# Performance work log

Measured on AMD Instinct MI355X. Metric: run time of the kernel, lower is better.

## Reference

```python
import jax, jax.numpy as jnp
import numpy as np

B, T, C = 8, 2048, 1024
HS, HO = 64, 64  # head_size, head_output_dim

def setup_inputs() -> dict:
    key = jax.random.key(0)
    k1, k2, k3, k4 = jax.random.split(key, 4)
    x = jax.random.normal(k1, (B, T, C), dtype=jnp.float32)
    Wk = jax.random.normal(k2, (HS, C), dtype=jnp.float32) * (C ** -0.5)
    Wq = jax.random.normal(k3, (HS, C), dtype=jnp.float32) * (C ** -0.5)
    Wv = jax.random.normal(k4, (HO, C), dtype=jnp.float32) * (C ** -0.5)
    return {"x": x, "Wk": Wk, "Wq": Wq, "Wv": Wv}

def reference(x, Wk, Wq, Wv):
    Bx, Tx, Cx = x.shape
    k = jnp.einsum('btc,hc->bth', x, Wk)  # [B,T,HS]
    q = jnp.einsum('btc,hc->bth', x, Wq)  # [B,T,HS]
    v = jnp.einsum('btc,oc->bto', x, Wv)  # [B,T,HO]
    scores = jnp.einsum('bth,bsh->bts', q, k)  # [B,T,T]
    causal = jnp.tril(jnp.ones((Tx, Tx), dtype=bool))
    scores = jnp.where(causal, scores, -jnp.inf)
    # original scales AFTER masking; -inf * scale stays -inf, same softmax result
    weights = jax.nn.softmax(scores * (HS ** -0.5), axis=-1)
    return jnp.einsum('bts,bso->bto', weights, v)
```

## Files before the change

kernel.cpp:

```cpp
#include <hip/hip_runtime.h>
#include <hip/hip_bf16.h>

typedef __attribute__((ext_vector_type(8))) short short8;
typedef __attribute__((ext_vector_type(4))) float float4v;

#define LOG2E 1.44269504088896340736f

typedef __attribute__((address_space(1))) const unsigned int gu32;
typedef __attribute__((address_space(3))) unsigned int su32;

__device__ __forceinline__ unsigned short f2bf(float f) {
    unsigned int u = __float_as_uint(f);
    unsigned int r = (u + 0x7fffu + ((u >> 16) & 1u)) >> 16;
    return (unsigned short)r;
}

__global__ void wconv_kernel(const float* __restrict__ Wk, const float* __restrict__ Wq,
                             const float* __restrict__ Wv, unsigned short* __restrict__ Wb) {
    int i = blockIdx.x * 256 + threadIdx.x;
    if (i >= 192 * 1024) return;
    float v;
    if (i < 65536)       v = Wk[i];
    else if (i < 131072) v = Wq[i - 65536];
    else                 v = Wv[i - 131072];
    Wb[i] = f2bf(v);
}

__global__ __launch_bounds__(256) void proj_kernel(
    const float* __restrict__ x, const unsigned short* __restrict__ Wb,
    unsigned short* __restrict__ qs, unsigned short* __restrict__ ks,
    unsigned short* __restrict__ vT) {
    __shared__ unsigned short Bl[3][12288];

    const int tid  = threadIdx.x;
    const int lane = tid & 63;
    const int wave = tid >> 6;
    const int rg   = wave & 1;
    const int g    = wave >> 1;
    const int quad = lane >> 4;
    const int l16  = lane & 15;
    const int t0   = blockIdx.x * 32;

    const int srow_in = lane >> 3;
    const int csrc    = (lane & 7) ^ srow_in;

    const int rowA = t0 + rg * 16 + l16;
    const float* xr = x + (size_t)rowA * 1024;

    float4v acc[6];
#pragma unroll
    for (int n = 0; n < 6; n++) acc[n] = (float4v){0.f, 0.f, 0.f, 0.f};

#define STAGE_B(BUF, KN)                                                          \
    {                                                                             \
        _Pragma("unroll")                                                         \
        for (int i = 0; i < 6; i++) {                                             \
            const int region = wave * 6 + i;                                      \
            const int rowg   = region * 8 + srow_in;                              \
            const unsigned short* src = Wb + (size_t)rowg * 1024 + (KN) + csrc * 8; \
            __builtin_amdgcn_global_load_lds((gu32*)src,                          \
                                             (su32*)&Bl[BUF][region * 512],       \
                                             16, 0, 0);                           \
        }                                                                         \
    }

#define LOAD_A(DST, KN)                                             \
    {                                                               \
        DST[0] = *(const float4v*)(xr + (KN) + quad * 8);           \
        DST[1] = *(const float4v*)(xr + (KN) + quad * 8 + 4);       \
        DST[2] = *(const float4v*)(xr + (KN) + 32 + quad * 8);      \
        DST[3] = *(const float4v*)(xr + (KN) + 32 + quad * 8 + 4);  \
    }

    STAGE_B(0, 0)
    asm volatile("" ::: "memory");
    float4v a0[4], a1[4];
    LOAD_A(a0, 0)
    asm volatile("" ::: "memory");
    STAGE_B(1, 64)
    asm volatile("" ::: "memory");
    LOAD_A(a1, 64)

    const int swz = l16 & 7;

#pragma unroll
    for (int kt = 0; kt < 16; kt++) {
        __builtin_amdgcn_sched_barrier(0);
        if (kt < 15) {
            asm volatile("s_waitcnt vmcnt(10)" ::: "memory");
        } else {
            asm volatile("s_waitcnt vmcnt(0)" ::: "memory");
        }
        __builtin_amdgcn_s_barrier();
        if (kt < 14) {
            STAGE_B((kt + 2) % 3, (kt + 2) * 64)
            asm volatile("" ::: "memory");
        }
        float4v an[4];
        if (kt < 14) {
            LOAD_A(an, (kt + 2) * 64)
            asm volatile("" ::: "memory");
        }
        const unsigned short* Bc = Bl[kt % 3];
#pragma unroll
        for (int kc = 0; kc < 2; kc++) {
            short8 af;
#pragma unroll
            for (int j = 0; j < 4; j++) af[j] = (short)f2bf(a0[kc * 2][j]);
#pragma unroll
            for (int j = 0; j < 4; j++) af[4 + j] = (short)f2bf(a0[kc * 2 + 1][j]);
#pragma unroll
            for (int n = 0; n < 6; n++) {
                const int row  = (g * 6 + n) * 16 + l16;
                const int coff = ((kc * 4 + quad) ^ swz) * 8;
                const short8 bf = *(const short8*)&Bc[row * 64 + coff];
                acc[n] = __builtin_amdgcn_mfma_f32_16x16x32_bf16(af, bf, acc[n], 0, 0, 0);
            }
        }
        if (kt < 14) {
#pragma unroll
            for (int i = 0; i < 4; i++) { a0[i] = a1[i]; a1[i] = an[i]; }
        } else if (kt < 15) {
#pragma unroll
            for (int i = 0; i < 4; i++) a0[i] = a1[i];
        }
    }
#undef STAGE_B
#undef LOAD_A

    const int rowD = t0 + rg * 16 + quad * 4;
#pragma unroll
    for (int r = 0; r < 4; r++) {
        const int t = rowD + r;
        const int b = t >> 11, tt = t & 2047;
        if (g == 0) {
#pragma unroll
            for (int n = 0; n < 4; n++)
                ks[(size_t)t * 64 + n * 16 + l16] = f2bf(acc[n][r]);
#pragma unroll
            for (int n = 4; n < 6; n++)
                qs[(size_t)t * 64 + (n - 4) * 16 + l16] = f2bf(acc[n][r] * 0.125f);
        } else {
#pragma unroll
            for (int n = 0; n < 2; n++)
                qs[(size_t)t * 64 + (n + 2) * 16 + l16] = f2bf(acc[n][r] * 0.125f);
#pragma unroll
            for (int n = 2; n < 6; n++)
                vT[(size_t)b * 131072 + (size_t)((n - 2) * 16 + l16) * 2048 + tt] = f2bf(acc[n][r]);
        }
    }
}

__global__ __launch_bounds__(256) void attn_kernel(
    const unsigned short* __restrict__ qs, const unsigned short* __restrict__ ks,
    const unsigned short* __restrict__ vT, float* __restrict__ out) {
    __shared__ unsigned short Kl[4 * 64 * 72];
    __shared__ unsigned short Vl[64 * 264];
    __shared__ unsigned short P[4][16 * 72];
    __shared__ float Ll[4][16];
    float* Of = (float*)Kl;

    const int tid  = threadIdx.x;
    const int lane = tid & 63;
    const int wave = tid >> 6;
    const int quad = lane >> 4;
    const int l16  = lane & 15;
    const int bx   = blockIdx.x;
    const int b    = bx & 7;
    const int i    = bx >> 3;
    const int qt   = (i & 1) ? (127 - (i >> 1)) : (i >> 1);
    const int t0   = qt * 16;

    const unsigned short* qb = qs + (size_t)b * 131072;
    const unsigned short* kb = ks + (size_t)b * 131072;
    const unsigned short* vb = vT + (size_t)b * 131072;

    const int ksr = tid >> 3;
    const int ksc = (tid & 7) * 8;
    const int vsr = tid >> 5;
    const int vsc = (tid & 31) * 8;

    const int qrow = t0 + l16;
    const short8 qf0 = *(const short8*)(qb + (size_t)qrow * 64 + quad * 8);
    const short8 qf1 = *(const short8*)(qb + (size_t)qrow * 64 + 32 + quad * 8);

    float4v o[4];
#pragma unroll
    for (int ot = 0; ot < 4; ot++) o[ot] = (float4v){0.f, 0.f, 0.f, 0.f};
    float lpart = 0.f;

    const int nkb  = (qt >> 2) + 1;
    const int nsup = (nkb + 3) >> 2;

    for (int s = 0; s < nsup; s++) {
        const int key0 = s * 256;
        __syncthreads();
#pragma unroll
        for (int i2 = 0; i2 < 8; i2++) {
            int kr = key0 + i2 * 32 + ksr; kr = kr < 2047 ? kr : 2047;
            *(short8*)&Kl[(i2 * 32 + ksr) * 72 + ksc] = *(const short8*)(kb + (size_t)kr * 64 + ksc);
        }
#pragma unroll
        for (int i2 = 0; i2 < 8; i2++) {
            const int orow = i2 * 8 + vsr;
            int kc2 = key0 + vsc; kc2 = kc2 < 2040 ? kc2 : 2040;
            *(short8*)&Vl[orow * 264 + vsc] = *(const short8*)(vb + (size_t)orow * 2048 + kc2);
        }
        __syncthreads();

        const int jt = s * 4 + wave;
        if (jt < nkb) {
            const int kbase = wave * 64;
            float4v sv[4];
#pragma unroll
            for (int kt = 0; kt < 4; kt++) {
                const short8 ka = *(const short8*)&Kl[(kbase + kt * 16 + l16) * 72 + quad * 8];
                const short8 kc = *(const short8*)&Kl[(kbase + kt * 16 + l16) * 72 + 32 + quad * 8];
                float4v z = (float4v){0.f, 0.f, 0.f, 0.f};
                z = __builtin_amdgcn_mfma_f32_16x16x32_bf16(ka, qf0, z, 0, 0, 0);
                sv[kt] = __builtin_amdgcn_mfma_f32_16x16x32_bf16(kc, qf1, z, 0, 0, 0);
            }
            if (jt == nkb - 1) {
#pragma unroll
                for (int kt = 0; kt < 4; kt++)
#pragma unroll
                    for (int r = 0; r < 4; r++)
                        if (jt * 64 + kt * 16 + quad * 4 + r > qrow) sv[kt][r] = -1e30f;
            }
#pragma unroll
            for (int kt = 0; kt < 4; kt++) {
                float p0 = exp2f(sv[kt][0] * LOG2E);
                float p1 = exp2f(sv[kt][1] * LOG2E);
                float p2 = exp2f(sv[kt][2] * LOG2E);
                float p3 = exp2f(sv[kt][3] * LOG2E);
                lpart += (p0 + p1) + (p2 + p3);
                unsigned int lo = (unsigned int)f2bf(p0) | ((unsigned int)f2bf(p1) << 16);
                unsigned int hi = (unsigned int)f2bf(p2) | ((unsigned int)f2bf(p3) << 16);
                unsigned long long w = ((unsigned long long)hi << 32) | lo;
                *(unsigned long long*)&P[wave][l16 * 72 + kt * 16 + quad * 4] = w;
            }
#pragma unroll
            for (int kc = 0; kc < 2; kc++) {
                const short8 pf = *(const short8*)&P[wave][l16 * 72 + kc * 32 + quad * 8];
#pragma unroll
                for (int ot = 0; ot < 4; ot++) {
                    const short8 vf = *(const short8*)&Vl[(ot * 16 + l16) * 264 + wave * 64 + kc * 32 + quad * 8];
                    o[ot] = __builtin_amdgcn_mfma_f32_16x16x32_bf16(pf, vf, o[ot], 0, 0, 0);
                }
            }
        }
    }

    lpart += __shfl_xor(lpart, 16);
    lpart += __shfl_xor(lpart, 32);
    __syncthreads();
#pragma unroll
    for (int r = 0; r < 4; r++)
#pragma unroll
        for (int ot = 0; ot < 4; ot++)
            Of[wave * 1088 + (quad * 4 + r) * 68 + ot * 16 + l16] = o[ot][r];
    if (lane < 16) Ll[wave][lane] = lpart;
    __syncthreads();

    {
        const int row = tid >> 4;
        const int c0  = (tid & 15) * 4;
        const float lsum = Ll[0][row] + Ll[1][row] + Ll[2][row] + Ll[3][row];
        float4v v0 = *(const float4v*)&Of[0 * 1088 + row * 68 + c0];
        float4v v1 = *(const float4v*)&Of[1 * 1088 + row * 68 + c0];
        float4v v2 = *(const float4v*)&Of[2 * 1088 + row * 68 + c0];
        float4v v3 = *(const float4v*)&Of[3 * 1088 + row * 68 + c0];
        float4v res;
        const float inv = 1.0f / lsum;
#pragma unroll
        for (int j = 0; j < 4; j++)
            res[j] = ((v0[j] + v1[j]) + (v2[j] + v3[j])) * inv;
        float* ob = out + (size_t)b * 131072 + (size_t)(t0 + row) * 64 + c0;
        *(float4v*)ob = res;
    }
}

extern "C" void kernel_launch(void* const* d_in, const int* in_sizes, int n_in,
                              void* d_out, int out_size, void* d_ws, size_t ws_size,
                              hipStream_t stream) {
    const float* x  = (const float*)d_in[0];
    const float* Wk = (const float*)d_in[1];
    const float* Wq = (const float*)d_in[2];
    const float* Wv = (const float*)d_in[3];
    float* out = (float*)d_out;

    unsigned short* Wb  = (unsigned short*)d_ws;
    unsigned short* qsb = (unsigned short*)((char*)d_ws + 393216);
    unsigned short* ksb = qsb + 1048576;
    unsigned short* vTb = ksb + 1048576;

    hipLaunchKernelGGL(wconv_kernel, dim3(768), dim3(256), 0, stream, Wk, Wq, Wv, Wb);
    hipLaunchKernelGGL(proj_kernel, dim3(512), dim3(256), 0, stream, x, Wb, qsb, ksb, vTb);
    hipLaunchKernelGGL(attn_kernel, dim3(1024), dim3(256), 0, stream, qsb, ksb, vTb, out);
}
```

Before: 154.2 us.

## Stage projection operands through registers into double-buffered LDS with cooperative A tile

Replaces the direct global-to-LDS async loads of the weight tile (triple buffer) with register-staged loads written into a double-buffered LDS tile. The x activations are now loaded cooperatively, converted to bf16 once per element, and stored into a swizzled LDS tile. Previously each wave converted its own fp32 fragments, so conversion work was duplicated across the wave groups. The change trades the async-copy path and deeper prefetch for fewer redundant conversions and fewer global reads of x. It adds register pressure and an extra LDS write/read round trip per k-step.

```diff
diff --git a/kernel.cpp b/kernel.cpp
--- a/kernel.cpp
+++ b/kernel.cpp
@@ -5,9 +5,6 @@
 typedef __attribute__((ext_vector_type(4))) float float4v;
 
 #define LOG2E 1.44269504088896340736f
-
-typedef __attribute__((address_space(1))) const unsigned int gu32;
-typedef __attribute__((address_space(3))) unsigned int su32;
 
 __device__ __forceinline__ unsigned short f2bf(float f) {
     unsigned int u = __float_as_uint(f);
@@ -30,7 +27,8 @@
     const float* __restrict__ x, const unsigned short* __restrict__ Wb,
     unsigned short* __restrict__ qs, unsigned short* __restrict__ ks,
     unsigned short* __restrict__ vT) {
-    __shared__ unsigned short Bl[3][12288];
+    __shared__ unsigned short Bl[2][12288];
+    __shared__ unsigned short Al[2][2048];
 
     const int tid  = threadIdx.x;
     const int lane = tid & 63;
@@ -41,92 +39,111 @@
     const int l16  = lane & 15;
     const int t0   = blockIdx.x * 32;
 
-    const int srow_in = lane >> 3;
-    const int csrc    = (lane & 7) ^ srow_in;
-
-    const int rowA = t0 + rg * 16 + l16;
-    const float* xr = x + (size_t)rowA * 1024;
+    const int brow_in = lane >> 3;
+    const int bchunk  = lane & 7;
+    const int bwchunk = bchunk ^ brow_in;
+
+    const int ar = tid >> 3;
+    const int ak = tid & 7;
+    const float* xsrc = x + (size_t)(t0 + ar) * 1024 + ak * 8;
+    const int awoff = ar * 64 + ((ak ^ (ar & 7)) * 8);
+
+    const int arow = rg * 16 + l16;
+    const int swz  = l16 & 7;
 
     float4v acc[6];
 #pragma unroll
     for (int n = 0; n < 6; n++) acc[n] = (float4v){0.f, 0.f, 0.f, 0.f};
 
-#define STAGE_B(BUF, KN)                                                          \
+#define STAGE_LOAD_B(REG, KN)                                                     \
     {                                                                             \
         _Pragma("unroll")                                                         \
         for (int i = 0; i < 6; i++) {                                             \
-            const int region = wave * 6 + i;                                      \
-            const int rowg   = region * 8 + srow_in;                              \
-            const unsigned short* src = Wb + (size_t)rowg * 1024 + (KN) + csrc * 8; \
-            __builtin_amdgcn_global_load_lds((gu32*)src,                          \
-                                             (su32*)&Bl[BUF][region * 512],       \
-                                             16, 0, 0);                           \
+            const int rowg = (wave * 6 + i) * 8 + brow_in;                        \
+            REG[i] = *(const short8*)(Wb + (size_t)rowg * 1024 + (KN) + bchunk * 8); \
         }                                                                         \
     }
 
-#define LOAD_A(DST, KN)                                             \
-    {                                                               \
-        DST[0] = *(const float4v*)(xr + (KN) + quad * 8);           \
-        DST[1] = *(const float4v*)(xr + (KN) + quad * 8 + 4);       \
-        DST[2] = *(const float4v*)(xr + (KN) + 32 + quad * 8);      \
-        DST[3] = *(const float4v*)(xr + (KN) + 32 + quad * 8 + 4);  \
-    }
-
-    STAGE_B(0, 0)
+#define STAGE_WRITE_B(BUF, REG)                                                   \
+    {                                                                             \
+        _Pragma("unroll")                                                         \
+        for (int i = 0; i < 6; i++)                                               \
+            *(short8*)&Bl[BUF][(wave * 6 + i) * 512 + brow_in * 64 + bwchunk * 8] = REG[i]; \
+    }
+
+#define LOAD_A_G(F0, F1, KN)                              \
+    {                                                     \
+        F0 = *(const float4v*)(xsrc + (KN));              \
+        F1 = *(const float4v*)(xsrc + (KN) + 4);          \
+    }
+
+#define STAGE_WRITE_A(BUF, F0, F1)                        \
+    {                                                     \
+        short8 w;                                         \
+        _Pragma("unroll")                                 \
+        for (int j = 0; j < 4; j++) {                     \
+            w[j]     = (short)f2bf(F0[j]);                \
+            w[4 + j] = (short)f2bf(F1[j]);                \
+        }                                                 \
+        *(short8*)&Al[BUF][awoff] = w;                    \
+    }
+
+    short8 breg[6];
+    float4v aS[2][2];
+    float4v a0f0, a0f1;
+    STAGE_LOAD_B(breg, 0)
     asm volatile("" ::: "memory");
-    float4v a0[4], a1[4];
-    LOAD_A(a0, 0)
+    LOAD_A_G(a0f0, a0f1, 0)
     asm volatile("" ::: "memory");
-    STAGE_B(1, 64)
-    asm volatile("" ::: "memory");
-    LOAD_A(a1, 64)
-
-    const int swz = l16 & 7;
+    LOAD_A_G(aS[1][0], aS[1][1], 64)
+    asm volatile("s_waitcnt vmcnt(2)" ::: "memory");
+    STAGE_WRITE_B(0, breg)
+    STAGE_WRITE_A(0, a0f0, a0f1)
+    asm volatile("s_waitcnt lgkmcnt(0)" ::: "memory");
+    __builtin_amdgcn_s_barrier();
 
 #pragma unroll
     for (int kt = 0; kt < 16; kt++) {
         __builtin_amdgcn_sched_barrier(0);
         if (kt < 15) {
-            asm volatile("s_waitcnt vmcnt(10)" ::: "memory");
-        } else {
-            asm volatile("s_waitcnt vmcnt(0)" ::: "memory");
-        }
-        __builtin_amdgcn_s_barrier();
+            STAGE_LOAD_B(breg, (kt + 1) * 64)
+        }
+        asm volatile("" ::: "memory");
         if (kt < 14) {
-            STAGE_B((kt + 2) % 3, (kt + 2) * 64)
-            asm volatile("" ::: "memory");
-        }
-        float4v an[4];
-        if (kt < 14) {
-            LOAD_A(an, (kt + 2) * 64)
-            asm volatile("" ::: "memory");
-        }
-        const unsigned short* Bc = Bl[kt % 3];
+            LOAD_A_G(aS[kt & 1][0], aS[kt & 1][1], (kt + 2) * 64)
+        }
+        asm volatile("" ::: "memory");
+
+        const unsigned short* Bc = Bl[kt & 1];
+        const unsigned short* Ac = Al[kt & 1];
 #pragma unroll
         for (int kc = 0; kc < 2; kc++) {
-            short8 af;
-#pragma unroll
-            for (int j = 0; j < 4; j++) af[j] = (short)f2bf(a0[kc * 2][j]);
-#pragma unroll
-            for (int j = 0; j < 4; j++) af[4 + j] = (short)f2bf(a0[kc * 2 + 1][j]);
+            const int coff = ((kc * 4 + quad) ^ swz) * 8;
+            const short8 af = *(const short8*)&Ac[arow * 64 + coff];
 #pragma unroll
             for (int n = 0; n < 6; n++) {
-                const int row  = (g * 6 + n) * 16 + l16;
-                const int coff = ((kc * 4 + quad) ^ swz) * 8;
+                const int row = (g * 6 + n) * 16 + l16;
                 const short8 bf = *(const short8*)&Bc[row * 64 + coff];
                 acc[n] = __builtin_amdgcn_mfma_f32_16x16x32_bf16(af, bf, acc[n], 0, 0, 0);
             }
         }
-        if (kt < 14) {
-#pragma unroll
-            for (int i = 0; i < 4; i++) { a0[i] = a1[i]; a1[i] = an[i]; }
-        } else if (kt < 15) {
-#pragma unroll
-            for (int i = 0; i < 4; i++) a0[i] = a1[i];
-        }
-    }
-#undef STAGE_B
-#undef LOAD_A
+
+        if (kt < 15) {
+            if (kt < 14) {
+                asm volatile("s_waitcnt vmcnt(2)" ::: "memory");
+            } else {
+                asm volatile("s_waitcnt vmcnt(0)" ::: "memory");
+            }
+            STAGE_WRITE_B((kt + 1) & 1, breg)
+            STAGE_WRITE_A((kt + 1) & 1, aS[(kt + 1) & 1][0], aS[(kt + 1) & 1][1])
+            asm volatile("s_waitcnt lgkmcnt(0)" ::: "memory");
+            __builtin_amdgcn_s_barrier();
+        }
+    }
+#undef STAGE_LOAD_B
+#undef STAGE_WRITE_B
+#undef LOAD_A_G
+#undef STAGE_WRITE_A
 
     const int rowD = t0 + rg * 16 + quad * 4;
 #pragma unroll
```

Result: faster. 142.4 us (-7.7%).
